# Performance work log

Hardware: AMD Instinct MI355X
Metric: run time of the kernel (lower is better)

The kernel has to match this reference:

```python
import jax, jax.numpy as jnp
import numpy as np

B, S, D, NH = 4, 2048, 512, 8
HD = D // NH
SCALING = HD ** -0.5


def setup_inputs() -> dict:
    key = jax.random.key(0)
    ks = jax.random.split(key, 8)
    w_std = (2.0 / (D + D)) ** 0.5  # xavier_uniform-ish scale
    inp = {
        "query": jax.random.normal(ks[0], (B, S, D), jnp.float32),
        "key": jax.random.normal(ks[1], (B, S, D), jnp.float32),
        "value": jax.random.normal(ks[2], (B, S, D), jnp.float32),
        "key_mask": jnp.ones((B, S), dtype=bool),
        "attn_mask": jnp.tril(jnp.ones((S, S), dtype=bool)),  # causal, per docstring
        "Wq": jax.random.normal(ks[3], (D, D), jnp.float32) * w_std,
        "bq": jnp.zeros((D,), jnp.float32),
        "Wk": jax.random.normal(ks[4], (D, D), jnp.float32) * w_std,
        "bk": jnp.zeros((D,), jnp.float32),
        "Wv": jax.random.normal(ks[5], (D, D), jnp.float32) * w_std,
        "bv": jnp.zeros((D,), jnp.float32),
        "Wo": jax.random.normal(ks[6], (D, D), jnp.float32) * w_std,
        "bo": jnp.zeros((D,), jnp.float32),
    }
    return inp


def reference(query, key, value, key_mask, attn_mask, Wq, bq, Wk, bk, Wv, bv, Wo, bo):
    b, q_len, d = query.shape
    k_len = key.shape[1]
    # projections (nn.Linear: x @ W.T + b)
    q = (query @ Wq.T + bq) * SCALING
    k = key @ Wk.T + bk
    v = value @ Wv.T + bv
    q = q.reshape(b, q_len, NH, HD)
    k = k.reshape(b, k_len, NH, HD)
    v = v.reshape(b, k_len, NH, HD)
    # scores: [b, q, k, n]
    attn = jnp.einsum('bqnh,bknh->bqkn', q, k)
    # key_mask: 1 = attend; masked_fill(~mask, -inf)
    attn = jnp.where(key_mask[:, None, :, None], attn, -jnp.inf)
    # attn_mask: [q, k], 1 = attend
    attn = jnp.where(attn_mask[None, :, :, None], attn, -jnp.inf)
    attn = jax.nn.softmax(attn, axis=2)
    # dropout p=0.0 in eval -> identity
    out = jnp.einsum('bqkn,bknh->bqnh', attn, v)
    out = out.reshape(b, q_len, d)
    out = out @ Wo.T + bo
    return (out, attn)
```

## Files before the change

### kernel.cpp

```cpp
#include <hip/hip_runtime.h>


typedef short bf8 __attribute__((ext_vector_type(8)));
typedef short bf4 __attribute__((ext_vector_type(4)));
typedef float f4  __attribute__((ext_vector_type(4)));

#define MFMA16(a, b, c) __builtin_amdgcn_mfma_f32_16x16x32_bf16(a, b, c, 0, 0, 0)

static __device__ __forceinline__ short f2bf(float x) {
  unsigned u = __builtin_bit_cast(unsigned, x);
  unsigned r = (u + 0x7fffu + ((u >> 16) & 1u)) >> 16;
  return (short)r;
}
static __device__ __forceinline__ f4 zero4() { f4 z = {0.f, 0.f, 0.f, 0.f}; return z; }

union SmemQKV {
  struct { short As[128 * 40]; short Bs[128 * 40]; } st;
  short Ct[128 * 136];
};

__global__ __launch_bounds__(256, 3) void gemm_qkv(const float* __restrict__ Aq,
                                                   const float* __restrict__ Ak,
                                                   const float* __restrict__ Av,
                                                   const float* __restrict__ Wq,
                                                   const float* __restrict__ Wk,
                                                   const float* __restrict__ Wv,
                                                   const float* __restrict__ bq,
                                                   const float* __restrict__ bk,
                                                   const float* __restrict__ bv,
                                                   short* __restrict__ Qo,
                                                   short* __restrict__ Ko,
                                                   short* __restrict__ Vo) {
  __shared__ SmemQKV u;
  const int z = blockIdx.z;
  const float* A = (z == 0) ? Aq : (z == 1) ? Ak : Av;
  const float* W = (z == 0) ? Wq : (z == 1) ? Wk : Wv;
  const float* bias = (z == 0) ? bq : (z == 1) ? bk : bv;
  short* out = (z == 0) ? Qo : (z == 1) ? Ko : Vo;
  const float scale = (z == 0) ? 0.125f : 1.0f;

  const int tid = threadIdx.x;
  const int wave = tid >> 6, lane = tid & 63, quad = lane >> 4, col = lane & 15;
  const int m0 = blockIdx.y * 128, n0 = blockIdx.x * 128;
  const int row_off = (wave >> 1) * 64, col_off = (wave & 1) * 64;

  f4 acc[4][4];
#pragma unroll
  for (int i = 0; i < 4; ++i)
#pragma unroll
    for (int j = 0; j < 4; ++j) acc[i][j] = zero4();

  float bvv[4];
#pragma unroll
  for (int nt = 0; nt < 4; ++nt) bvv[nt] = bias[n0 + col_off + nt * 16 + col];

  for (int k0 = 0; k0 < 512; k0 += 32) {
#pragma unroll
    for (int i = 0; i < 4; ++i) {
      int c = i * 256 + tid;
      int r = c >> 3, cc = (c & 7) * 4;
      f4 v = *(const f4*)(A + (size_t)(m0 + r) * 512 + k0 + cc);
      bf4 s = {f2bf(v[0]), f2bf(v[1]), f2bf(v[2]), f2bf(v[3])};
      *(bf4*)&u.st.As[r * 40 + cc] = s;
      f4 w = *(const f4*)(W + (size_t)(n0 + r) * 512 + k0 + cc);
      bf4 sw = {f2bf(w[0]), f2bf(w[1]), f2bf(w[2]), f2bf(w[3])};
      *(bf4*)&u.st.Bs[r * 40 + cc] = sw;
    }
    __syncthreads();
    bf8 af[4], bw[4];
#pragma unroll
    for (int mt = 0; mt < 4; ++mt) af[mt] = *(const bf8*)&u.st.As[(row_off + mt * 16 + col) * 40 + quad * 8];
#pragma unroll
    for (int nt = 0; nt < 4; ++nt) bw[nt] = *(const bf8*)&u.st.Bs[(col_off + nt * 16 + col) * 40 + quad * 8];
#pragma unroll
    for (int mt = 0; mt < 4; ++mt)
#pragma unroll
      for (int nt = 0; nt < 4; ++nt) acc[mt][nt] = MFMA16(af[mt], bw[nt], acc[mt][nt]);
    __syncthreads();
  }

  if (z != 2) {
#pragma unroll
    for (int mt = 0; mt < 4; ++mt)
#pragma unroll
      for (int nt = 0; nt < 4; ++nt)
#pragma unroll
        for (int r = 0; r < 4; ++r)
          u.Ct[(row_off + mt * 16 + quad * 4 + r) * 136 + col_off + nt * 16 + col] =
              f2bf((acc[mt][nt][r] + bvv[nt]) * scale);
  } else {
#pragma unroll
    for (int mt = 0; mt < 4; ++mt)
#pragma unroll
      for (int nt = 0; nt < 4; ++nt) {
        bf4 s = {f2bf(acc[mt][nt][0] + bvv[nt]), f2bf(acc[mt][nt][1] + bvv[nt]),
                 f2bf(acc[mt][nt][2] + bvv[nt]), f2bf(acc[mt][nt][3] + bvv[nt])};
        *(bf4*)&u.Ct[(col_off + nt * 16 + col) * 136 + row_off + mt * 16 + quad * 4] = s;
      }
  }
  __syncthreads();
#pragma unroll
  for (int it = 0; it < 8; ++it) {
    int c = it * 256 + tid;
    if (z != 2) {
      int row = c >> 4, ch = (c & 15) * 8;
      int m = m0 + row, bb = m >> 11, sidx = m & 2047;
      int cg = n0 + ch, n = cg >> 6, h = cg & 63;
      bf8 v = *(const bf8*)&u.Ct[row * 136 + ch];
      *(bf8*)(out + ((size_t)((bb * 8 + n) * 2048 + sidx)) * 64 + h) = v;
    } else {
      int j = c >> 4, sc8 = (c & 15) * 8;
      int cg = n0 + j, n = cg >> 6, h = cg & 63;
      int m = m0 + sc8, bb = m >> 11, srow = m & 2047;
      bf8 v = *(const bf8*)&u.Ct[j * 136 + sc8];
      *(bf8*)(out + ((size_t)((bb * 8 + n) * 64 + h)) * 2048 + srow) = v;
    }
  }
}

__global__ __launch_bounds__(256, 2) void gemm_out(const short* __restrict__ A,
                                                   const float* __restrict__ W,
                                                   const float* __restrict__ bias,
                                                   float* __restrict__ out) {
  __shared__ short As[128 * 40];
  __shared__ short Bs[128 * 40];
  const int tid = threadIdx.x;
  const int wave = tid >> 6, lane = tid & 63, quad = lane >> 4, col = lane & 15;
  const int m0 = blockIdx.y * 128, n0 = blockIdx.x * 128;
  const int row_off = (wave >> 1) * 64, col_off = (wave & 1) * 64;

  f4 acc[4][4];
#pragma unroll
  for (int i = 0; i < 4; ++i)
#pragma unroll
    for (int j = 0; j < 4; ++j) acc[i][j] = zero4();

  float bv[4];
#pragma unroll
  for (int nt = 0; nt < 4; ++nt) bv[nt] = bias[n0 + col_off + nt * 16 + col];

  for (int k0 = 0; k0 < 512; k0 += 32) {
#pragma unroll
    for (int i = 0; i < 4; ++i) {
      int c = i * 256 + tid;
      int r = c >> 3, cc = (c & 7) * 4;
      *(bf4*)&As[r * 40 + cc] = *(const bf4*)(A + (size_t)(m0 + r) * 512 + k0 + cc);
      f4 w = *(const f4*)(W + (size_t)(n0 + r) * 512 + k0 + cc);
      bf4 sw = {f2bf(w[0]), f2bf(w[1]), f2bf(w[2]), f2bf(w[3])};
      *(bf4*)&Bs[r * 40 + cc] = sw;
    }
    __syncthreads();
    bf8 af[4], bw[4];
#pragma unroll
    for (int mt = 0; mt < 4; ++mt) af[mt] = *(const bf8*)&As[(row_off + mt * 16 + col) * 40 + quad * 8];
#pragma unroll
    for (int nt = 0; nt < 4; ++nt) bw[nt] = *(const bf8*)&Bs[(col_off + nt * 16 + col) * 40 + quad * 8];
#pragma unroll
    for (int mt = 0; mt < 4; ++mt)
#pragma unroll
      for (int nt = 0; nt < 4; ++nt) acc[mt][nt] = MFMA16(af[mt], bw[nt], acc[mt][nt]);
    __syncthreads();
  }

#pragma unroll
  for (int mt = 0; mt < 4; ++mt)
#pragma unroll
    for (int nt = 0; nt < 4; ++nt) {
      int rb = m0 + row_off + mt * 16 + quad * 4;
      int cg = n0 + col_off + nt * 16 + col;
#pragma unroll
      for (int r = 0; r < 4; ++r) out[(size_t)(rb + r) * 512 + cg] = acc[mt][nt][r] + bv[nt];
    }
}

#define SLAB 1092
#define PBUF (8 * SLAB)

__global__ __launch_bounds__(512, 4) void attn_k(const short* __restrict__ Q,
                                                 const short* __restrict__ K,
                                                 const short* __restrict__ Vt,
                                                 short* __restrict__ O,
                                                 float* __restrict__ attn) {
  __shared__ float Pl[2 * PBUF];
  __shared__ float rl_s[128];
  const int tid = threadIdx.x;
  const int wv = tid >> 6, lane = tid & 63, quad = lane >> 4, col = lane & 15;
  const int bid = blockIdx.x;
  const int b = bid & 3;
  const int q0 = (127 - (bid >> 2)) * 16;
  const int q_hi = q0 + 15;
  const int nsteps = (q_hi >> 6) + 1;

  const int klim = nsteps << 6;
  if (klim < 2048) {
    int nf4 = (2048 - klim) * 2;
#pragma unroll 1
    for (int qq = 0; qq < 16; ++qq) {
      f4* dst = (f4*)(attn + ((size_t)(b * 2048 + q0 + qq) * 2048 + klim) * 8);
      for (int i = tid; i < nf4; i += 512) __builtin_nontemporal_store(zero4(), dst + i);
    }
  }

  const size_t hb = (size_t)(b * 8 + wv) * 2048;
  const bf8 aq0 = *(const bf8*)(Q + (hb + q0 + col) * 64 + quad * 8);
  const bf8 aq1 = *(const bf8*)(Q + (hb + q0 + col) * 64 + 32 + quad * 8);

  float rl[4] = {0.f, 0.f, 0.f, 0.f};
  for (int ks = 0; ks < nsteps; ++ks) {
    int k0 = ks << 6;
    bf8 kf0[4], kf1[4];
#pragma unroll
    for (int kt = 0; kt < 4; ++kt) {
      int kb = k0 + kt * 16;
      if (kb <= q_hi) {
        const short* kp = K + (hb + kb + col) * 64 + quad * 8;
        kf0[kt] = *(const bf8*)kp;
        kf1[kt] = *(const bf8*)(kp + 32);
      }
    }
#pragma unroll
    for (int kt = 0; kt < 4; ++kt) {
      int kb = k0 + kt * 16;
      if (kb <= q_hi) {
        f4 sc = zero4();
        sc = MFMA16(aq0, kf0[kt], sc);
        sc = MFMA16(aq1, kf1[kt], sc);
        if (kb + 15 <= q0) {
#pragma unroll
          for (int r = 0; r < 4; ++r) rl[r] += __expf(sc[r]);
        } else {
          int kg = kb + col;
#pragma unroll
          for (int r = 0; r < 4; ++r) rl[r] += (kg <= q0 + quad * 4 + r) ? __expf(sc[r]) : 0.f;
        }
      }
    }
  }
#pragma unroll
  for (int r = 0; r < 4; ++r) {
    float v = rl[r];
    v += __shfl_xor(v, 1);
    v += __shfl_xor(v, 2);
    v += __shfl_xor(v, 4);
    v += __shfl_xor(v, 8);
    rl[r] = 1.0f / v;
  }
  if (col == 0) {
#pragma unroll
    for (int r = 0; r < 4; ++r) rl_s[wv * 16 + quad * 4 + r] = rl[r];
  }
  __syncthreads();

  const int gq = tid >> 5, gc0 = tid & 31;
  const int gnb = (gc0 & 1) * 4, gk0 = gc0 >> 1;
  float rl8[4];
#pragma unroll
  for (int j = 0; j < 4; ++j) rl8[j] = rl_s[(gnb + j) * 16 + gq];

  f4 oacc[4];
#pragma unroll
  for (int t = 0; t < 4; ++t) oacc[t] = zero4();

  for (int ks = 0; ks < nsteps; ++ks) {
    int k0 = ks << 6;
    float* buf = Pl + (ks & 1) * PBUF;
    bf8 kf0[4], kf1[4];
#pragma unroll
    for (int kt = 0; kt < 4; ++kt) {
      int kb = k0 + kt * 16;
      if (kb <= q_hi) {
        const short* kp = K + (hb + kb + col) * 64 + quad * 8;
        kf0[kt] = *(const bf8*)kp;
        kf1[kt] = *(const bf8*)(kp + 32);
      }
    }
#pragma unroll
    for (int kt = 0; kt < 4; ++kt) {
      int kb = k0 + kt * 16;
      f4 p = zero4();
      if (kb <= q_hi) {
        f4 sc = zero4();
        sc = MFMA16(aq0, kf0[kt], sc);
        sc = MFMA16(aq1, kf1[kt], sc);
        if (kb + 15 <= q0) {
#pragma unroll
          for (int r = 0; r < 4; ++r) p[r] = __expf(sc[r]);
        } else {
          int kg = kb + col;
#pragma unroll
          for (int r = 0; r < 4; ++r) p[r] = (kg <= q0 + quad * 4 + r) ? __expf(sc[r]) : 0.f;
        }
      }
      float* wp = buf + wv * SLAB + (quad * 4) * 68 + kt * 16 + col;
#pragma unroll
      for (int r = 0; r < 4; ++r) wp[r * 68] = p[r];
    }
    __syncthreads();

    bf8 vr[8];
#pragma unroll
    for (int kk = 0; kk < 2; ++kk)
#pragma unroll
      for (int t = 0; t < 4; ++t)
        vr[kk * 4 + t] =
            *(const bf8*)(Vt + ((size_t)((b * 8 + wv) * 64 + t * 16 + col)) * 2048 + k0 + kk * 32 + quad * 8);

    {
      float* dst = attn + ((size_t)(b * 2048 + q0 + gq) * 2048 + k0) * 8;
      const float* base = Pl + (ks & 1) * PBUF + gq * 68;
#pragma unroll
      for (int i = 0; i < 4; ++i) {
        int k = gk0 + 16 * i;
        f4 v;
#pragma unroll
        for (int j = 0; j < 4; ++j) v[j] = base[(gnb + j) * SLAB + k] * rl8[j];
        __builtin_nontemporal_store(v, (f4*)(dst + k * 8 + gnb));
      }
    }
#pragma unroll
    for (int kk = 0; kk < 2; ++kk) {
      const float* pp = buf + wv * SLAB + col * 68 + kk * 32 + quad * 8;
      f4 a0 = *(const f4*)pp;
      f4 a1 = *(const f4*)(pp + 4);
      bf8 ap = {f2bf(a0[0]), f2bf(a0[1]), f2bf(a0[2]), f2bf(a0[3]),
                f2bf(a1[0]), f2bf(a1[1]), f2bf(a1[2]), f2bf(a1[3])};
#pragma unroll
      for (int t = 0; t < 4; ++t) oacc[t] = MFMA16(ap, vr[kk * 4 + t], oacc[t]);
    }
  }

  __syncthreads();
#pragma unroll
  for (int t = 0; t < 4; ++t)
#pragma unroll
    for (int r = 0; r < 4; ++r)
      Pl[(quad * 4 + r) * 516 + wv * 64 + t * 16 + col] = oacc[t][r] * rl[r];
  __syncthreads();
  {
    const float* src = Pl + gq * 516;
    short* dst = O + (size_t)(b * 2048 + q0 + gq) * 512;
#pragma unroll
    for (int i = 0; i < 4; ++i) {
      int cc = (gc0 + 32 * i) * 4;
      f4 v = *(const f4*)(src + cc);
      bf4 s = {f2bf(v[0]), f2bf(v[1]), f2bf(v[2]), f2bf(v[3])};
      *(bf4*)(dst + cc) = s;
    }
  }
}

extern "C" void kernel_launch(void* const* d_in, const int* in_sizes, int n_in,
                              void* d_out, int out_size, void* d_ws, size_t ws_size,
                              hipStream_t stream) {
  const float* query = (const float*)d_in[0];
  const float* key = (const float*)d_in[1];
  const float* value = (const float*)d_in[2];
  const float* Wq = (const float*)d_in[5];
  const float* bq = (const float*)d_in[6];
  const float* Wk = (const float*)d_in[7];
  const float* bk = (const float*)d_in[8];
  const float* Wv = (const float*)d_in[9];
  const float* bv = (const float*)d_in[10];
  const float* Wo = (const float*)d_in[11];
  const float* bo = (const float*)d_in[12];

  char* ws = (char*)d_ws;
  const size_t MB8 = (size_t)8 * 1024 * 1024;
  short* Qb = (short*)(ws);
  short* Kb = (short*)(ws + MB8);
  short* Vt = (short*)(ws + 2 * MB8);
  short* Ob = (short*)(ws + 3 * MB8);

  float* out = (float*)d_out;
  float* attn = out + (size_t)4 * 2048 * 512;

  gemm_qkv<<<dim3(4, 64, 3), 256, 0, stream>>>(query, key, value, Wq, Wk, Wv, bq, bk, bv, Qb, Kb, Vt);
  attn_k<<<512, 512, 0, stream>>>(Qb, Kb, Vt, Ob, attn);
  gemm_out<<<dim3(4, 64), 256, 0, stream>>>(Ob, Wo, bo, out);
}
```

Measured before the change: 851.4 us.

## Pre-convert inputs to bf16 and stage GEMM tiles with direct global-to-LDS loads

```diff
diff --git a/kernel.cpp b/kernel.cpp
--- a/kernel.cpp
+++ b/kernel.cpp
@@ -14,17 +14,47 @@
 }
 static __device__ __forceinline__ f4 zero4() { f4 z = {0.f, 0.f, 0.f, 0.f}; return z; }
 
+static __device__ __forceinline__ void gload16(const short* g, short* l) {
+  __builtin_amdgcn_global_load_lds((const __attribute__((address_space(1))) unsigned*)g,
+                                   (__attribute__((address_space(3))) unsigned*)l, 16, 0, 0);
+}
+
+__global__ __launch_bounds__(256) void convert_bf16(const float* __restrict__ q,
+                                                    const float* __restrict__ k,
+                                                    const float* __restrict__ v,
+                                                    const float* __restrict__ wq,
+                                                    const float* __restrict__ wk,
+                                                    const float* __restrict__ wv,
+                                                    const float* __restrict__ wo,
+                                                    short* __restrict__ qc, short* __restrict__ kc,
+                                                    short* __restrict__ vc, short* __restrict__ wqc,
+                                                    short* __restrict__ wkc, short* __restrict__ wvc,
+                                                    short* __restrict__ woc) {
+  const int z = blockIdx.z;
+  const float* src = (z == 0) ? q : (z == 1) ? k : (z == 2) ? v
+                   : (z == 3) ? wq : (z == 4) ? wk : (z == 5) ? wv : wo;
+  short* dst = (z == 0) ? qc : (z == 1) ? kc : (z == 2) ? vc
+             : (z == 3) ? wqc : (z == 4) ? wkc : (z == 5) ? wvc : woc;
+  const int n4 = (z < 3) ? (4 * 2048 * 512 / 4) : (512 * 512 / 4);
+  const int stride = gridDim.x * blockDim.x;
+  for (int i = blockIdx.x * blockDim.x + threadIdx.x; i < n4; i += stride) {
+    f4 x = ((const f4*)src)[i];
+    bf4 y = {f2bf(x[0]), f2bf(x[1]), f2bf(x[2]), f2bf(x[3])};
+    ((bf4*)dst)[i] = y;
+  }
+}
+
 union SmemQKV {
-  struct { short As[128 * 40]; short Bs[128 * 40]; } st;
+  struct { short As[128 * 32]; short Bs[128 * 32]; } st;
   short Ct[128 * 136];
 };
 
-__global__ __launch_bounds__(256, 3) void gemm_qkv(const float* __restrict__ Aq,
-                                                   const float* __restrict__ Ak,
-                                                   const float* __restrict__ Av,
-                                                   const float* __restrict__ Wq,
-                                                   const float* __restrict__ Wk,
-                                                   const float* __restrict__ Wv,
+__global__ __launch_bounds__(256, 3) void gemm_qkv(const short* __restrict__ Aq,
+                                                   const short* __restrict__ Ak,
+                                                   const short* __restrict__ Av,
+                                                   const short* __restrict__ Wq,
+                                                   const short* __restrict__ Wk,
+                                                   const short* __restrict__ Wv,
                                                    const float* __restrict__ bq,
                                                    const float* __restrict__ bk,
                                                    const float* __restrict__ bv,
@@ -33,8 +63,8 @@
                                                    short* __restrict__ Vo) {
   __shared__ SmemQKV u;
   const int z = blockIdx.z;
-  const float* A = (z == 0) ? Aq : (z == 1) ? Ak : Av;
-  const float* W = (z == 0) ? Wq : (z == 1) ? Wk : Wv;
+  const short* A = (z == 0) ? Aq : (z == 1) ? Ak : Av;
+  const short* W = (z == 0) ? Wq : (z == 1) ? Wk : Wv;
   const float* bias = (z == 0) ? bq : (z == 1) ? bk : bv;
   short* out = (z == 0) ? Qo : (z == 1) ? Ko : Vo;
   const float scale = (z == 0) ? 0.125f : 1.0f;
@@ -54,24 +84,22 @@
 #pragma unroll
   for (int nt = 0; nt < 4; ++nt) bvv[nt] = bias[n0 + col_off + nt * 16 + col];
 
+  const int off0 = wave * 1024 + lane * 16;
+  const int r0 = off0 >> 6, ce0 = (off0 & 63) >> 1;
+
   for (int k0 = 0; k0 < 512; k0 += 32) {
 #pragma unroll
-    for (int i = 0; i < 4; ++i) {
-      int c = i * 256 + tid;
-      int r = c >> 3, cc = (c & 7) * 4;
-      f4 v = *(const f4*)(A + (size_t)(m0 + r) * 512 + k0 + cc);
-      bf4 s = {f2bf(v[0]), f2bf(v[1]), f2bf(v[2]), f2bf(v[3])};
-      *(bf4*)&u.st.As[r * 40 + cc] = s;
-      f4 w = *(const f4*)(W + (size_t)(n0 + r) * 512 + k0 + cc);
-      bf4 sw = {f2bf(w[0]), f2bf(w[1]), f2bf(w[2]), f2bf(w[3])};
-      *(bf4*)&u.st.Bs[r * 40 + cc] = sw;
+    for (int s = 0; s < 2; ++s) {
+      int r = r0 + s * 64;
+      gload16(A + (size_t)(m0 + r) * 512 + k0 + ce0, &u.st.As[(s * 4096 + off0) >> 1]);
+      gload16(W + (size_t)(n0 + r) * 512 + k0 + ce0, &u.st.Bs[(s * 4096 + off0) >> 1]);
     }
     __syncthreads();
     bf8 af[4], bw[4];
 #pragma unroll
-    for (int mt = 0; mt < 4; ++mt) af[mt] = *(const bf8*)&u.st.As[(row_off + mt * 16 + col) * 40 + quad * 8];
-#pragma unroll
-    for (int nt = 0; nt < 4; ++nt) bw[nt] = *(const bf8*)&u.st.Bs[(col_off + nt * 16 + col) * 40 + quad * 8];
+    for (int mt = 0; mt < 4; ++mt) af[mt] = *(const bf8*)&u.st.As[(row_off + mt * 16 + col) * 32 + quad * 8];
+#pragma unroll
+    for (int nt = 0; nt < 4; ++nt) bw[nt] = *(const bf8*)&u.st.Bs[(col_off + nt * 16 + col) * 32 + quad * 8];
 #pragma unroll
     for (int mt = 0; mt < 4; ++mt)
 #pragma unroll
@@ -119,11 +147,11 @@
 }
 
 __global__ __launch_bounds__(256, 2) void gemm_out(const short* __restrict__ A,
-                                                   const float* __restrict__ W,
+                                                   const short* __restrict__ W,
                                                    const float* __restrict__ bias,
                                                    float* __restrict__ out) {
-  __shared__ short As[128 * 40];
-  __shared__ short Bs[128 * 40];
+  __shared__ short As[128 * 32];
+  __shared__ short Bs[128 * 32];
   const int tid = threadIdx.x;
   const int wave = tid >> 6, lane = tid & 63, quad = lane >> 4, col = lane & 15;
   const int m0 = blockIdx.y * 128, n0 = blockIdx.x * 128;
@@ -139,22 +167,22 @@
 #pragma unroll
   for (int nt = 0; nt < 4; ++nt) bv[nt] = bias[n0 + col_off + nt * 16 + col];
 
+  const int off0 = wave * 1024 + lane * 16;
+  const int r0 = off0 >> 6, ce0 = (off0 & 63) >> 1;
+
   for (int k0 = 0; k0 < 512; k0 += 32) {
 #pragma unroll
-    for (int i = 0; i < 4; ++i) {
-      int c = i * 256 + tid;
-      int r = c >> 3, cc = (c & 7) * 4;
-      *(bf4*)&As[r * 40 + cc] = *(const bf4*)(A + (size_t)(m0 + r) * 512 + k0 + cc);
-      f4 w = *(const f4*)(W + (size_t)(n0 + r) * 512 + k0 + cc);
-      bf4 sw = {f2bf(w[0]), f2bf(w[1]), f2bf(w[2]), f2bf(w[3])};
-      *(bf4*)&Bs[r * 40 + cc] = sw;
+    for (int s = 0; s < 2; ++s) {
+      int r = r0 + s * 64;
+      gload16(A + (size_t)(m0 + r) * 512 + k0 + ce0, &As[(s * 4096 + off0) >> 1]);
+      gload16(W + (size_t)(n0 + r) * 512 + k0 + ce0, &Bs[(s * 4096 + off0) >> 1]);
     }
     __syncthreads();
     bf8 af[4], bw[4];
 #pragma unroll
-    for (int mt = 0; mt < 4; ++mt) af[mt] = *(const bf8*)&As[(row_off + mt * 16 + col) * 40 + quad * 8];
-#pragma unroll
-    for (int nt = 0; nt < 4; ++nt) bw[nt] = *(const bf8*)&Bs[(col_off + nt * 16 + col) * 40 + quad * 8];
+    for (int mt = 0; mt < 4; ++mt) af[mt] = *(const bf8*)&As[(row_off + mt * 16 + col) * 32 + quad * 8];
+#pragma unroll
+    for (int nt = 0; nt < 4; ++nt) bw[nt] = *(const bf8*)&Bs[(col_off + nt * 16 + col) * 32 + quad * 8];
 #pragma unroll
     for (int mt = 0; mt < 4; ++mt)
 #pragma unroll
@@ -365,16 +393,25 @@
   const float* bo = (const float*)d_in[12];
 
   char* ws = (char*)d_ws;
-  const size_t MB8 = (size_t)8 * 1024 * 1024;
+  const size_t MB = (size_t)1024 * 1024;
   short* Qb = (short*)(ws);
-  short* Kb = (short*)(ws + MB8);
-  short* Vt = (short*)(ws + 2 * MB8);
-  short* Ob = (short*)(ws + 3 * MB8);
+  short* Kb = (short*)(ws + 8 * MB);
+  short* Vt = (short*)(ws + 16 * MB);
+  short* Ob = (short*)(ws + 24 * MB);
+  short* Qc = (short*)(ws + 32 * MB);
+  short* Kc = (short*)(ws + 40 * MB);
+  short* Vc = (short*)(ws + 48 * MB);
+  short* Wqc = (short*)(ws + 56 * MB);
+  short* Wkc = (short*)(ws + 56 * MB + 512 * 1024);
+  short* Wvc = (short*)(ws + 57 * MB);
+  short* Woc = (short*)(ws + 57 * MB + 512 * 1024);
 
   float* out = (float*)d_out;
   float* attn = out + (size_t)4 * 2048 * 512;
 
-  gemm_qkv<<<dim3(4, 64, 3), 256, 0, stream>>>(query, key, value, Wq, Wk, Wv, bq, bk, bv, Qb, Kb, Vt);
+  convert_bf16<<<dim3(512, 1, 7), 256, 0, stream>>>(query, key, value, Wq, Wk, Wv, Wo,
+                                                    Qc, Kc, Vc, Wqc, Wkc, Wvc, Woc);
+  gemm_qkv<<<dim3(4, 64, 3), 256, 0, stream>>>(Qc, Kc, Vc, Wqc, Wkc, Wvc, bq, bk, bv, Qb, Kb, Vt);
   attn_k<<<512, 512, 0, stream>>>(Qb, Kb, Vt, Ob, attn);
-  gemm_out<<<dim3(4, 64), 256, 0, stream>>>(Ob, Wo, bo, out);
-}
+  gemm_out<<<dim3(4, 64), 256, 0, stream>>>(Ob, Woc, bo, out);
+}
```

After: 841.8 us. No clear change (-1.1%).
